# Kernel tuning notes

Measured on AMD Instinct MI355X. Metric: run time of the kernel, lower is better.

## Reference

```python
import jax, jax.numpy as jnp
import numpy as np


def _gcn_layer(x, W, b, src, dst, n_dst):
    """DGL GraphConv with norm='both': D_dst^{-1/2} A D_src^{-1/2} X W + b."""
    n_src = x.shape[0]
    ones = jnp.ones(src.shape[0], dtype=x.dtype)
    out_deg = jnp.clip(jax.ops.segment_sum(ones, src, num_segments=n_src), 1.0)
    in_deg = jnp.clip(jax.ops.segment_sum(ones, dst, num_segments=n_dst), 1.0)
    xn = x * (out_deg ** -0.5)[:, None]          # [n_src, F] source-side norm
    agg = jax.ops.segment_sum(xn[src], dst, num_segments=n_dst)  # sparse SpMM
    agg = agg * (in_deg ** -0.5)[:, None]        # dest-side norm
    return agg @ W + b


def setup_inputs() -> dict:
    key = jax.random.key(0)
    ks = jax.random.split(key, 9)
    N0, N1, N2 = 200000, 100000, 50000
    E1, E2 = 1600000, 800000
    F_in, F_hid, F_out = 128, 256, 128
    x = jax.random.normal(ks[0], (N0, F_in), dtype=jnp.float32)
    src1 = jax.random.randint(ks[1], (E1,), 0, N0, dtype=jnp.int32)
    dst1 = jax.random.randint(ks[2], (E1,), 0, N1, dtype=jnp.int32)
    src2 = jax.random.randint(ks[3], (E2,), 0, N1, dtype=jnp.int32)
    dst2 = jax.random.randint(ks[4], (E2,), 0, N2, dtype=jnp.int32)
    # Glorot-uniform weights like dgl GraphConv reset_parameters
    lim1 = (6.0 / (F_in + F_hid)) ** 0.5
    lim2 = (6.0 / (F_hid + F_out)) ** 0.5
    W1 = jax.random.uniform(ks[5], (F_in, F_hid), jnp.float32, -lim1, lim1)
    b1 = jnp.zeros((F_hid,), jnp.float32)
    W2 = jax.random.uniform(ks[6], (F_hid, F_out), jnp.float32, -lim2, lim2)
    b2 = jnp.zeros((F_out,), jnp.float32)
    return {"x": x, "W1": W1, "b1": b1, "W2": W2, "b2": b2,
            "src1": src1, "dst1": dst1, "src2": src2, "dst2": dst2,
            "n_dst1": N1, "n_dst2": N2}


def reference(x, W1, b1, W2, b2, src1, dst1, src2, dst2, n_dst1, n_dst2):
    h = jax.nn.relu(_gcn_layer(x, W1, b1, src1, dst1, n_dst1))
    out = jax.nn.relu(_gcn_layer(h, W2, b2, src2, dst2, n_dst2))
    return out
```

## Files before the change

kernel.cpp:

```cpp
#include <hip/hip_runtime.h>
#include <hip/hip_bf16.h>

#define F1 128
#define F2 256
#define F3 128
#define CAP 64

#define NB1D 391
#define NB2D 196
#define NB1S 782
#define NB2S 391
#define CAPD 4608
#define CAPS 2432
#define GD1 0
#define GD2 391
#define GS1 587
#define GS2 1369

typedef __attribute__((ext_vector_type(8))) short bf16x8;
typedef __attribute__((ext_vector_type(4))) float f32x4;
typedef __attribute__((ext_vector_type(4))) unsigned int u32x4;

__device__ inline float bf2f(unsigned short u) {
    return __uint_as_float(((unsigned int)u) << 16);
}
__device__ inline unsigned short f2bf(float f) {
    __hip_bfloat16 b = __float2bfloat16(f);
    return *reinterpret_cast<unsigned short*>(&b);
}
__device__ inline unsigned int pack2(float lo, float hi) {
    return ((unsigned int)f2bf(hi) << 16) | f2bf(lo);
}

#define ACC_ROW(u, c)                                   \
    acc[0] = fmaf(c, bf2f(u.x & 0xffff), acc[0]);       \
    acc[1] = fmaf(c, bf2f(u.x >> 16), acc[1]);          \
    acc[2] = fmaf(c, bf2f(u.y & 0xffff), acc[2]);       \
    acc[3] = fmaf(c, bf2f(u.y >> 16), acc[3]);          \
    acc[4] = fmaf(c, bf2f(u.z & 0xffff), acc[4]);       \
    acc[5] = fmaf(c, bf2f(u.z >> 16), acc[5]);          \
    acc[6] = fmaf(c, bf2f(u.w & 0xffff), acc[6]);       \
    acc[7] = fmaf(c, bf2f(u.w >> 16), acc[7]);

__global__ __launch_bounds__(1024) void scatter_build(
    const int* __restrict__ src1, const int* __restrict__ dst1,
    const int* __restrict__ src2, const int* __restrict__ dst2,
    const float* __restrict__ x, const float* __restrict__ W1,
    const float* __restrict__ W2, int* __restrict__ gcnt,
    unsigned int* __restrict__ bkt_d1, unsigned int* __restrict__ bkt_d2,
    unsigned char* __restrict__ bkt_s1, unsigned char* __restrict__ bkt_s2,
    unsigned int* __restrict__ xn, unsigned short* __restrict__ Bp1,
    unsigned short* __restrict__ Bp2, int E1, int E2, int A1, int A2, int B3) {
    __shared__ int hist[1184];
    int b = blockIdx.x, t = threadIdx.x;

    if (b < A1 + A2) {
        const int L1 = (b < A1);
        const int* __restrict__ src = L1 ? src1 : src2;
        const int* __restrict__ dst = L1 ? dst1 : dst2;
        const int E = L1 ? E1 : E2;
        const int NBd = L1 ? NB1D : NB2D;
        const int NBs = L1 ? NB1S : NB2S;
        int* gd = gcnt + (L1 ? GD1 : GD2);
        int* gs = gcnt + (L1 ? GS1 : GS2);
        unsigned int* bd = L1 ? bkt_d1 : bkt_d2;
        unsigned char* bs = L1 ? bkt_s1 : bkt_s2;
        int* hd = hist;
        int* hs = hist + NBd;
        for (int i = t; i < NBd + NBs; i += 1024) hist[i] = 0;
        __syncthreads();
        int e0 = (L1 ? b : b - A1) * 8192;
        int se[8], de[8];
#pragma unroll
        for (int i = 0; i < 8; ++i) {
            int e = e0 + i * 1024 + t;
            se[i] = -1;
            de[i] = -1;
            if (e < E) {
                int s = src[e], d = dst[e];
                se[i] = s;
                de[i] = d;
                atomicAdd(&hd[d >> 8], 1);
                atomicAdd(&hs[s >> 8], 1);
            }
        }
        __syncthreads();
        for (int i = t; i < NBd; i += 1024) {
            int c = hd[i];
            hd[i] = c ? atomicAdd(&gd[i], c) : 0;
        }
        for (int i = t; i < NBs; i += 1024) {
            int c = hs[i];
            hs[i] = c ? atomicAdd(&gs[i], c) : 0;
        }
        __syncthreads();
#pragma unroll
        for (int i = 0; i < 8; ++i) {
            if (de[i] >= 0) {
                int s = se[i], d = de[i];
                int pd = atomicAdd(&hd[d >> 8], 1);
                if (pd < CAPD)
                    bd[(size_t)(d >> 8) * CAPD + pd] = ((unsigned int)s << 8) | (d & 255);
                int ps = atomicAdd(&hs[s >> 8], 1);
                if (ps < CAPS)
                    bs[(size_t)(s >> 8) * CAPS + ps] = (unsigned char)(s & 255);
            }
        }
    } else if (b < A1 + A2 + B3) {
        size_t tid = (size_t)(b - A1 - A2) * 1024 + t;
        const f32x4* xp = (const f32x4*)x;
        f32x4 a = __builtin_nontemporal_load(xp + tid * 2);
        f32x4 c = __builtin_nontemporal_load(xp + tid * 2 + 1);
        u32x4 o;
        o.x = pack2(a.x, a.y);
        o.y = pack2(a.z, a.w);
        o.z = pack2(c.x, c.y);
        o.w = pack2(c.z, c.w);
        ((u32x4*)xn)[tid] = o;
    } else {
        int w = b - (A1 + A2 + B3);
        int which = w >> 5;
        const float* W = which ? W2 : W1;
        unsigned short* out = which ? Bp2 : Bp1;
        int N = which ? F3 : F2;
        int idx = (w & 31) * 1024 + t;
        int k = idx / N, n = idx % N;
        unsigned short v = f2bf(W[idx]);
        int kt = k >> 5, q = (k >> 3) & 3, j = k & 7;
        int nt = n >> 4, lane = q * 16 + (n & 15);
        int NT = N >> 4;
        out[(((kt * NT + nt) * 64 + lane) << 3) + j] = v;
    }
}

__global__ __launch_bounds__(256) void bucket_build(
    const int* __restrict__ gcnt,
    const unsigned int* __restrict__ bkt_d1, const unsigned int* __restrict__ bkt_d2,
    const unsigned char* __restrict__ bkt_s1, const unsigned char* __restrict__ bkt_s2,
    int* __restrict__ csr1, int* __restrict__ cnt_in1, float* __restrict__ rs_in1,
    int* __restrict__ csr2, int* __restrict__ cnt_in2, float* __restrict__ rs_in2,
    float* __restrict__ rs_out1, float* __restrict__ rs_out2) {
    __shared__ int hist[256];
    int b = blockIdx.x, t = threadIdx.x;
    hist[t] = 0;
    __syncthreads();

    if (b < NB1D + NB2D) {
        const int L1 = (b < NB1D);
        int bb = L1 ? b : b - NB1D;
        const unsigned int* bkt = L1 ? bkt_d1 : bkt_d2;
        int* csr = L1 ? csr1 : csr2;
        int* cnt_in = L1 ? cnt_in1 : cnt_in2;
        float* rs_in = L1 ? rs_in1 : rs_in2;
        int Nd = L1 ? 100000 : 50000;
        int n = gcnt[(L1 ? GD1 : GD2) + bb];
        if (n > CAPD) n = CAPD;
        size_t base = (size_t)bb * CAPD;
        for (int i = t; i < n; i += 256) {
            unsigned int v = bkt[base + i];
            int d = v & 255, s = (int)(v >> 8);
            int pos = atomicAdd(&hist[d], 1);
            if (pos < CAP) csr[((size_t)(bb * 256 + d)) * CAP + pos] = s;
        }
        __syncthreads();
        int node = bb * 256 + t;
        if (node < Nd) {
            int c = hist[t];
            cnt_in[node] = c < CAP ? c : CAP;
            rs_in[node] = rsqrtf((float)(c < 1 ? 1 : c));
        }
    } else {
        const int L1 = (b < NB1D + NB2D + NB1S);
        int bb = L1 ? b - (NB1D + NB2D) : b - (NB1D + NB2D + NB1S);
        const unsigned char* bkt = L1 ? bkt_s1 : bkt_s2;
        float* rs_out = L1 ? rs_out1 : rs_out2;
        int Ns = L1 ? 200000 : 100000;
        int n = gcnt[(L1 ? GS1 : GS2) + bb];
        if (n > CAPS) n = CAPS;
        size_t base = (size_t)bb * CAPS;
        for (int i = t; i < n; i += 256) atomicAdd(&hist[bkt[base + i]], 1);
        __syncthreads();
        int node = bb * 256 + t;
        if (node < Ns) rs_out[node] = rsqrtf((float)(hist[t] < 1 ? 1 : hist[t]));
    }
}

__global__ __launch_bounds__(256) void agg128_kernel(
    const unsigned int* __restrict__ X, const int* __restrict__ csr,
    const int* __restrict__ cnt, const float* __restrict__ rs_src,
    unsigned int* __restrict__ out, int ndst) {
    int wave = (int)((blockIdx.x * blockDim.x + threadIdx.x) >> 6);
    int lane = threadIdx.x & 63;
    if (wave >= ndst) return;
    size_t base = (size_t)wave * CAP;
    int len = cnt[wave];
    int sl = 0;
    float clv = 0.f;
    if (lane < len) {
        sl = csr[base + lane];
        clv = rs_src[sl];
    }
    int eg = lane >> 4, fs = lane & 15;
    float acc[8];
#pragma unroll
    for (int i = 0; i < 8; ++i) acc[i] = 0.f;
    for (int j = 0; j < len; j += 16) {
        int jA = j + eg, jB = j + 4 + eg, jC = j + 8 + eg, jD = j + 12 + eg;
        int sA = __shfl(sl, jA);
        int sB = __shfl(sl, jB);
        int sC = __shfl(sl, jC);
        int sD = __shfl(sl, jD);
        float cA = __shfl(clv, jA);
        float cB = __shfl(clv, jB);
        float cC = __shfl(clv, jC);
        float cD = __shfl(clv, jD);
        u32x4 uA = *(const u32x4*)(X + (size_t)sA * 64 + (fs << 2));
        u32x4 uB = *(const u32x4*)(X + (size_t)sB * 64 + (fs << 2));
        u32x4 uC = *(const u32x4*)(X + (size_t)sC * 64 + (fs << 2));
        u32x4 uD = *(const u32x4*)(X + (size_t)sD * 64 + (fs << 2));
        ACC_ROW(uA, cA)
        ACC_ROW(uB, cB)
        ACC_ROW(uC, cC)
        ACC_ROW(uD, cD)
    }
#pragma unroll
    for (int i = 0; i < 8; ++i) {
        acc[i] += __shfl_xor(acc[i], 16);
        acc[i] += __shfl_xor(acc[i], 32);
    }
    if (eg == 0) {
        u32x4 o;
        o.x = pack2(acc[0], acc[1]);
        o.y = pack2(acc[2], acc[3]);
        o.z = pack2(acc[4], acc[5]);
        o.w = pack2(acc[6], acc[7]);
        *((u32x4*)(out + (size_t)wave * 64) + fs) = o;
    }
}

__global__ __launch_bounds__(512) void gemm12(
    const unsigned short* __restrict__ A,
    const unsigned short* __restrict__ Bp1,
    const unsigned short* __restrict__ Bp2,
    const float* __restrict__ rs1, const float* __restrict__ rs2,
    const float* __restrict__ bias1,
    unsigned short* __restrict__ Y, int M) {
    __shared__ unsigned short Bs[32768];
    __shared__ unsigned short tmp[128][264];
    int lane = threadIdx.x & 63, wid = threadIdx.x >> 6;
    int t = threadIdx.x;
    int row0 = blockIdx.x * 128 + wid * 16;
    int q = lane >> 4, col = lane & 15;

#pragma unroll
    for (int i = 0; i < 8; ++i)
        ((u32x4*)Bs)[i * 512 + t] = ((const u32x4*)Bp1)[i * 512 + t];
    __syncthreads();

    int mload = row0 + col;
    if (mload > M - 1) mload = M - 1;
    const unsigned short* Arow = A + (size_t)mload * F1 + q * 8;
    f32x4 acc[16];
#pragma unroll
    for (int i = 0; i < 16; ++i) acc[i] = (f32x4){0.f, 0.f, 0.f, 0.f};
#pragma unroll
    for (int kt = 0; kt < 4; ++kt) {
        bf16x8 a = *(const bf16x8*)(Arow + kt * 32);
#pragma unroll
        for (int nt = 0; nt < 16; ++nt) {
            bf16x8 b = *(const bf16x8*)(Bs + (((kt * 16 + nt) * 64 + lane) << 3));
            acc[nt] = __builtin_amdgcn_mfma_f32_16x16x32_bf16(a, b, acc[nt], 0, 0, 0);
        }
    }
#pragma unroll
    for (int r = 0; r < 4; ++r) {
        int lrow = wid * 16 + q * 4 + r;
        int m = row0 + q * 4 + r;
        int mc = m < M ? m : M - 1;
        float s1 = rs1[mc], s2 = rs2[mc];
#pragma unroll
        for (int nt = 0; nt < 16; ++nt) {
            float v = fmaxf(fmaf(acc[nt][r], s1, bias1[nt * 16 + col]), 0.f) * s2;
            tmp[lrow][nt * 16 + col] = f2bf(v);
        }
    }
    __syncthreads();

#pragma unroll
    for (int i = 0; i < 8; ++i)
        ((u32x4*)Bs)[i * 512 + t] = ((const u32x4*)Bp2)[i * 512 + t];
    __syncthreads();

    f32x4 acc2[8];
#pragma unroll
    for (int i = 0; i < 8; ++i) acc2[i] = (f32x4){0.f, 0.f, 0.f, 0.f};
    const unsigned short* trow = &tmp[wid * 16 + col][q * 8];
#pragma unroll
    for (int kt = 0; kt < 8; ++kt) {
        bf16x8 a = *(const bf16x8*)(trow + kt * 32);
#pragma unroll
        for (int nt = 0; nt < 8; ++nt) {
            bf16x8 b = *(const bf16x8*)(Bs + (((kt * 8 + nt) * 64 + lane) << 3));
            acc2[nt] = __builtin_amdgcn_mfma_f32_16x16x32_bf16(a, b, acc2[nt], 0, 0, 0);
        }
    }
#pragma unroll
    for (int r = 0; r < 4; ++r) {
        int m = row0 + q * 4 + r;
        if (m >= M) continue;
#pragma unroll
        for (int nt = 0; nt < 8; ++nt)
            Y[(size_t)m * F3 + nt * 16 + col] = f2bf(acc2[nt][r]);
    }
}

__global__ __launch_bounds__(256) void agg_final(
    const unsigned int* __restrict__ Yv, const int* __restrict__ csr,
    const int* __restrict__ cnt, const float* __restrict__ rs_dst,
    const float* __restrict__ b2, float* __restrict__ out, int ndst) {
    int wave = (int)((blockIdx.x * blockDim.x + threadIdx.x) >> 6);
    int lane = threadIdx.x & 63;
    if (wave >= ndst) return;
    size_t base = (size_t)wave * CAP;
    int len = cnt[wave];
    int sl = 0;
    float clv = 0.f;
    if (lane < len) {
        sl = csr[base + lane];
        clv = 1.f;
    }
    int eg = lane >> 4, fs = lane & 15;
    float acc[8];
#pragma unroll
    for (int i = 0; i < 8; ++i) acc[i] = 0.f;
    for (int j = 0; j < len; j += 16) {
        int jA = j + eg, jB = j + 4 + eg, jC = j + 8 + eg, jD = j + 12 + eg;
        int sA = __shfl(sl, jA);
        int sB = __shfl(sl, jB);
        int sC = __shfl(sl, jC);
        int sD = __shfl(sl, jD);
        float cA = __shfl(clv, jA);
        float cB = __shfl(clv, jB);
        float cC = __shfl(clv, jC);
        float cD = __shfl(clv, jD);
        u32x4 uA = *(const u32x4*)(Yv + (size_t)sA * 64 + (fs << 2));
        u32x4 uB = *(const u32x4*)(Yv + (size_t)sB * 64 + (fs << 2));
        u32x4 uC = *(const u32x4*)(Yv + (size_t)sC * 64 + (fs << 2));
        u32x4 uD = *(const u32x4*)(Yv + (size_t)sD * 64 + (fs << 2));
        ACC_ROW(uA, cA)
        ACC_ROW(uB, cB)
        ACC_ROW(uC, cC)
        ACC_ROW(uD, cD)
    }
#pragma unroll
    for (int i = 0; i < 8; ++i) {
        acc[i] += __shfl_xor(acc[i], 16);
        acc[i] += __shfl_xor(acc[i], 32);
    }
    if (eg < 2) {
        float sc = rs_dst[wave];
        f32x4 bias = ((const f32x4*)b2)[(fs << 1) | eg];
        float v0 = eg ? acc[4] : acc[0];
        float v1 = eg ? acc[5] : acc[1];
        float v2 = eg ? acc[6] : acc[2];
        float v3 = eg ? acc[7] : acc[3];
        f32x4 o;
        o.x = fmaxf(fmaf(v0, sc, bias.x), 0.f);
        o.y = fmaxf(fmaf(v1, sc, bias.y), 0.f);
        o.z = fmaxf(fmaf(v2, sc, bias.z), 0.f);
        o.w = fmaxf(fmaf(v3, sc, bias.w), 0.f);
        __builtin_nontemporal_store(o, (f32x4*)out + (size_t)wave * 32 + (fs << 1) + eg);
    }
}

extern "C" void kernel_launch(void* const* d_in, const int* in_sizes, int n_in,
                              void* d_out, int out_size, void* d_ws, size_t ws_size,
                              hipStream_t stream) {
    const float* x  = (const float*)d_in[0];
    const float* W1 = (const float*)d_in[1];
    const float* b1 = (const float*)d_in[2];
    const float* W2 = (const float*)d_in[3];
    const float* b2 = (const float*)d_in[4];
    const int* src1 = (const int*)d_in[5];
    const int* dst1 = (const int*)d_in[6];
    const int* src2 = (const int*)d_in[7];
    const int* dst2 = (const int*)d_in[8];
    const int E1 = in_sizes[5], E2 = in_sizes[7];
    const int N0 = in_sizes[0] / F1;
    const int N1 = 100000, N2 = 50000;

    char* p = (char*)d_ws;
    int* gcnt = (int*)p; p += 2048 * 4;
    float* rs_out1 = (float*)p; p += (size_t)N0 * 4;
    float* rs_in1  = (float*)p; p += (size_t)N1 * 4;
    float* rs_out2 = (float*)p; p += (size_t)N1 * 4;
    float* rs_in2  = (float*)p; p += (size_t)N2 * 4;
    int* cnt_in1 = (int*)p; p += (size_t)N1 * 4;
    int* cnt_in2 = (int*)p; p += (size_t)N2 * 4;
    unsigned int* bkt_d1 = (unsigned int*)p; p += (size_t)NB1D * CAPD * 4;
    unsigned int* bkt_d2 = (unsigned int*)p; p += (size_t)NB2D * CAPD * 4;
    unsigned char* bkt_s1 = (unsigned char*)p; p += (size_t)NB1S * CAPS;
    unsigned char* bkt_s2 = (unsigned char*)p; p += (size_t)NB2S * CAPS;
    int* csr1 = (int*)p; p += (size_t)N1 * CAP * 4;
    int* csr2 = (int*)p; p += (size_t)N2 * CAP * 4;
    unsigned short* Bp1 = (unsigned short*)p; p += (size_t)F1 * F2 * 2;
    unsigned short* Bp2 = (unsigned short*)p; p += (size_t)F2 * F3 * 2;
    unsigned short* xn  = (unsigned short*)p; p += (size_t)N0 * F1 * 2;
    unsigned short* agg = (unsigned short*)p; p += (size_t)N1 * F1 * 2;
    unsigned short* y = xn;

    (void)hipMemsetAsync(gcnt, 0, 2048 * 4, stream);

    int A1 = (E1 + 8191) / 8192;
    int A2 = (E2 + 8191) / 8192;
    int B3 = N0 * F1 / 8 / 1024;
    scatter_build<<<A1 + A2 + B3 + 64, 1024, 0, stream>>>(
        src1, dst1, src2, dst2, x, W1, W2, gcnt,
        bkt_d1, bkt_d2, bkt_s1, bkt_s2,
        (unsigned int*)xn, Bp1, Bp2, E1, E2, A1, A2, B3);

    bucket_build<<<NB1D + NB2D + NB1S + NB2S, 256, 0, stream>>>(
        gcnt, bkt_d1, bkt_d2, bkt_s1, bkt_s2,
        csr1, cnt_in1, rs_in1, csr2, cnt_in2, rs_in2, rs_out1, rs_out2);

    agg128_kernel<<<(N1 + 3) / 4, 256, 0, stream>>>((const unsigned int*)xn, csr1,
                                                    cnt_in1, rs_out1,
                                                    (unsigned int*)agg, N1);

    gemm12<<<(N1 + 127) / 128, 512, 0, stream>>>(agg, Bp1, Bp2, rs_in1, rs_out2, b1, y, N1);

    agg_final<<<(N2 + 3) / 4, 256, 0, stream>>>((const unsigned int*)y, csr2, cnt_in2,
                                                rs_in2, b2, (float*)d_out, N2);
}
```

Measured before the change: 363.0 us.

## Build CSR directly with global atomics, drop bucket pass and precomputed norms

Replaces the two-pass bucketed graph build (shared-memory histograms, global bucket buffers, then a second bucket_build kernel) with a single pass that does per-node global atomicAdd for in-count, out-degree, and the CSR slot. Degree normalisation factors are now computed on the fly with rsqrtf from the raw integer counts inside the aggregation and GEMM kernels, so no rs_* arrays are written. agg_final points padded lanes at a zero row (row N1 of y, which gemm12 now zero-fills) instead of using a zero coefficient. This removes one kernel launch and the bucket round trip, but relies on heavily contended, scattered global atomics and random 4-byte CSR writes.

```diff
diff --git a/kernel.cpp b/kernel.cpp
--- a/kernel.cpp
+++ b/kernel.cpp
@@ -6,16 +6,7 @@
 #define F3 128
 #define CAP 64
 
-#define NB1D 391
-#define NB2D 196
-#define NB1S 782
-#define NB2S 391
-#define CAPD 4608
-#define CAPS 2432
-#define GD1 0
-#define GD2 391
-#define GS1 587
-#define GS2 1369
+#define YPAD 100096
 
 typedef __attribute__((ext_vector_type(8))) short bf16x8;
 typedef __attribute__((ext_vector_type(4))) float f32x4;
@@ -30,6 +21,9 @@
 }
 __device__ inline unsigned int pack2(float lo, float hi) {
     return ((unsigned int)f2bf(hi) << 16) | f2bf(lo);
+}
+__device__ inline float rsdeg(int c) {
+    return rsqrtf((float)(c < 1 ? 1 : c));
 }
 
 #define ACC_ROW(u, c)                                   \
@@ -42,16 +36,26 @@
     acc[6] = fmaf(c, bf2f(u.w & 0xffff), acc[6]);       \
     acc[7] = fmaf(c, bf2f(u.w >> 16), acc[7]);
 
+#define ACC_ROW_ADD(u)                          \
+    acc[0] += bf2f(u.x & 0xffff);               \
+    acc[1] += bf2f(u.x >> 16);                  \
+    acc[2] += bf2f(u.y & 0xffff);               \
+    acc[3] += bf2f(u.y >> 16);                  \
+    acc[4] += bf2f(u.z & 0xffff);               \
+    acc[5] += bf2f(u.z >> 16);                  \
+    acc[6] += bf2f(u.w & 0xffff);               \
+    acc[7] += bf2f(u.w >> 16);
+
 __global__ __launch_bounds__(1024) void scatter_build(
     const int* __restrict__ src1, const int* __restrict__ dst1,
     const int* __restrict__ src2, const int* __restrict__ dst2,
     const float* __restrict__ x, const float* __restrict__ W1,
-    const float* __restrict__ W2, int* __restrict__ gcnt,
-    unsigned int* __restrict__ bkt_d1, unsigned int* __restrict__ bkt_d2,
-    unsigned char* __restrict__ bkt_s1, unsigned char* __restrict__ bkt_s2,
+    const float* __restrict__ W2,
+    int* __restrict__ cnt1, int* __restrict__ outdeg1,
+    int* __restrict__ cnt2, int* __restrict__ outdeg2,
+    int* __restrict__ csr1, int* __restrict__ csr2,
     unsigned int* __restrict__ xn, unsigned short* __restrict__ Bp1,
     unsigned short* __restrict__ Bp2, int E1, int E2, int A1, int A2, int B3) {
-    __shared__ int hist[1184];
     int b = blockIdx.x, t = threadIdx.x;
 
     if (b < A1 + A2) {
@@ -59,51 +63,18 @@
         const int* __restrict__ src = L1 ? src1 : src2;
         const int* __restrict__ dst = L1 ? dst1 : dst2;
         const int E = L1 ? E1 : E2;
-        const int NBd = L1 ? NB1D : NB2D;
-        const int NBs = L1 ? NB1S : NB2S;
-        int* gd = gcnt + (L1 ? GD1 : GD2);
-        int* gs = gcnt + (L1 ? GS1 : GS2);
-        unsigned int* bd = L1 ? bkt_d1 : bkt_d2;
-        unsigned char* bs = L1 ? bkt_s1 : bkt_s2;
-        int* hd = hist;
-        int* hs = hist + NBd;
-        for (int i = t; i < NBd + NBs; i += 1024) hist[i] = 0;
-        __syncthreads();
+        int* cnt = L1 ? cnt1 : cnt2;
+        int* od  = L1 ? outdeg1 : outdeg2;
+        int* csr = L1 ? csr1 : csr2;
         int e0 = (L1 ? b : b - A1) * 8192;
-        int se[8], de[8];
-#pragma unroll
-        for (int i = 0; i < 8; ++i) {
-            int e = e0 + i * 1024 + t;
-            se[i] = -1;
-            de[i] = -1;
+#pragma unroll
+        for (int k = 0; k < 8; ++k) {
+            int e = e0 + k * 1024 + t;
             if (e < E) {
                 int s = src[e], d = dst[e];
-                se[i] = s;
-                de[i] = d;
-                atomicAdd(&hd[d >> 8], 1);
-                atomicAdd(&hs[s >> 8], 1);
-            }
-        }
-        __syncthreads();
-        for (int i = t; i < NBd; i += 1024) {
-            int c = hd[i];
-            hd[i] = c ? atomicAdd(&gd[i], c) : 0;
-        }
-        for (int i = t; i < NBs; i += 1024) {
-            int c = hs[i];
-            hs[i] = c ? atomicAdd(&gs[i], c) : 0;
-        }
-        __syncthreads();
-#pragma unroll
-        for (int i = 0; i < 8; ++i) {
-            if (de[i] >= 0) {
-                int s = se[i], d = de[i];
-                int pd = atomicAdd(&hd[d >> 8], 1);
-                if (pd < CAPD)
-                    bd[(size_t)(d >> 8) * CAPD + pd] = ((unsigned int)s << 8) | (d & 255);
-                int ps = atomicAdd(&hs[s >> 8], 1);
-                if (ps < CAPS)
-                    bs[(size_t)(s >> 8) * CAPS + ps] = (unsigned char)(s & 255);
+                atomicAdd(&od[s], 1);
+                int pos = atomicAdd(&cnt[d], 1);
+                if (pos < CAP) csr[(size_t)d * CAP + pos] = s;
             }
         }
     } else if (b < A1 + A2 + B3) {
@@ -133,72 +104,21 @@
     }
 }
 
-__global__ __launch_bounds__(256) void bucket_build(
-    const int* __restrict__ gcnt,
-    const unsigned int* __restrict__ bkt_d1, const unsigned int* __restrict__ bkt_d2,
-    const unsigned char* __restrict__ bkt_s1, const unsigned char* __restrict__ bkt_s2,
-    int* __restrict__ csr1, int* __restrict__ cnt_in1, float* __restrict__ rs_in1,
-    int* __restrict__ csr2, int* __restrict__ cnt_in2, float* __restrict__ rs_in2,
-    float* __restrict__ rs_out1, float* __restrict__ rs_out2) {
-    __shared__ int hist[256];
-    int b = blockIdx.x, t = threadIdx.x;
-    hist[t] = 0;
-    __syncthreads();
-
-    if (b < NB1D + NB2D) {
-        const int L1 = (b < NB1D);
-        int bb = L1 ? b : b - NB1D;
-        const unsigned int* bkt = L1 ? bkt_d1 : bkt_d2;
-        int* csr = L1 ? csr1 : csr2;
-        int* cnt_in = L1 ? cnt_in1 : cnt_in2;
-        float* rs_in = L1 ? rs_in1 : rs_in2;
-        int Nd = L1 ? 100000 : 50000;
-        int n = gcnt[(L1 ? GD1 : GD2) + bb];
-        if (n > CAPD) n = CAPD;
-        size_t base = (size_t)bb * CAPD;
-        for (int i = t; i < n; i += 256) {
-            unsigned int v = bkt[base + i];
-            int d = v & 255, s = (int)(v >> 8);
-            int pos = atomicAdd(&hist[d], 1);
-            if (pos < CAP) csr[((size_t)(bb * 256 + d)) * CAP + pos] = s;
-        }
-        __syncthreads();
-        int node = bb * 256 + t;
-        if (node < Nd) {
-            int c = hist[t];
-            cnt_in[node] = c < CAP ? c : CAP;
-            rs_in[node] = rsqrtf((float)(c < 1 ? 1 : c));
-        }
-    } else {
-        const int L1 = (b < NB1D + NB2D + NB1S);
-        int bb = L1 ? b - (NB1D + NB2D) : b - (NB1D + NB2D + NB1S);
-        const unsigned char* bkt = L1 ? bkt_s1 : bkt_s2;
-        float* rs_out = L1 ? rs_out1 : rs_out2;
-        int Ns = L1 ? 200000 : 100000;
-        int n = gcnt[(L1 ? GS1 : GS2) + bb];
-        if (n > CAPS) n = CAPS;
-        size_t base = (size_t)bb * CAPS;
-        for (int i = t; i < n; i += 256) atomicAdd(&hist[bkt[base + i]], 1);
-        __syncthreads();
-        int node = bb * 256 + t;
-        if (node < Ns) rs_out[node] = rsqrtf((float)(hist[t] < 1 ? 1 : hist[t]));
-    }
-}
-
 __global__ __launch_bounds__(256) void agg128_kernel(
     const unsigned int* __restrict__ X, const int* __restrict__ csr,
-    const int* __restrict__ cnt, const float* __restrict__ rs_src,
+    const int* __restrict__ cnt, const int* __restrict__ od_src,
     unsigned int* __restrict__ out, int ndst) {
     int wave = (int)((blockIdx.x * blockDim.x + threadIdx.x) >> 6);
     int lane = threadIdx.x & 63;
     if (wave >= ndst) return;
     size_t base = (size_t)wave * CAP;
     int len = cnt[wave];
+    if (len > CAP) len = CAP;
     int sl = 0;
     float clv = 0.f;
     if (lane < len) {
         sl = csr[base + lane];
-        clv = rs_src[sl];
+        clv = rsdeg(od_src[sl]);
     }
     int eg = lane >> 4, fs = lane & 15;
     float acc[8];
@@ -242,7 +162,7 @@
     const unsigned short* __restrict__ A,
     const unsigned short* __restrict__ Bp1,
     const unsigned short* __restrict__ Bp2,
-    const float* __restrict__ rs1, const float* __restrict__ rs2,
+    const int* __restrict__ cnt_in, const int* __restrict__ od2,
     const float* __restrict__ bias1,
     unsigned short* __restrict__ Y, int M) {
     __shared__ unsigned short Bs[32768];
@@ -268,8 +188,8 @@
         bf16x8 a = *(const bf16x8*)(Arow + kt * 32);
 #pragma unroll
         for (int nt = 0; nt < 16; ++nt) {
-            bf16x8 b = *(const bf16x8*)(Bs + (((kt * 16 + nt) * 64 + lane) << 3));
-            acc[nt] = __builtin_amdgcn_mfma_f32_16x16x32_bf16(a, b, acc[nt], 0, 0, 0);
+            bf16x8 bfr = *(const bf16x8*)(Bs + (((kt * 16 + nt) * 64 + lane) << 3));
+            acc[nt] = __builtin_amdgcn_mfma_f32_16x16x32_bf16(a, bfr, acc[nt], 0, 0, 0);
         }
     }
 #pragma unroll
@@ -277,7 +197,7 @@
         int lrow = wid * 16 + q * 4 + r;
         int m = row0 + q * 4 + r;
         int mc = m < M ? m : M - 1;
-        float s1 = rs1[mc], s2 = rs2[mc];
+        float s1 = rsdeg(cnt_in[mc]), s2 = rsdeg(od2[mc]);
 #pragma unroll
         for (int nt = 0; nt < 16; ++nt) {
             float v = fmaxf(fmaf(acc[nt][r], s1, bias1[nt * 16 + col]), 0.f) * s2;
@@ -300,35 +220,32 @@
         bf16x8 a = *(const bf16x8*)(trow + kt * 32);
 #pragma unroll
         for (int nt = 0; nt < 8; ++nt) {
-            bf16x8 b = *(const bf16x8*)(Bs + (((kt * 8 + nt) * 64 + lane) << 3));
-            acc2[nt] = __builtin_amdgcn_mfma_f32_16x16x32_bf16(a, b, acc2[nt], 0, 0, 0);
+            bf16x8 bfr = *(const bf16x8*)(Bs + (((kt * 8 + nt) * 64 + lane) << 3));
+            acc2[nt] = __builtin_amdgcn_mfma_f32_16x16x32_bf16(a, bfr, acc2[nt], 0, 0, 0);
         }
     }
 #pragma unroll
     for (int r = 0; r < 4; ++r) {
         int m = row0 + q * 4 + r;
-        if (m >= M) continue;
+        int live = m < M;
 #pragma unroll
         for (int nt = 0; nt < 8; ++nt)
-            Y[(size_t)m * F3 + nt * 16 + col] = f2bf(acc2[nt][r]);
+            Y[(size_t)m * F3 + nt * 16 + col] = live ? f2bf(acc2[nt][r]) : (unsigned short)0;
     }
 }
 
 __global__ __launch_bounds__(256) void agg_final(
     const unsigned int* __restrict__ Yv, const int* __restrict__ csr,
-    const int* __restrict__ cnt, const float* __restrict__ rs_dst,
-    const float* __restrict__ b2, float* __restrict__ out, int ndst) {
+    const int* __restrict__ cnt, const float* __restrict__ b2,
+    float* __restrict__ out, int ndst, int zrow) {
     int wave = (int)((blockIdx.x * blockDim.x + threadIdx.x) >> 6);
     int lane = threadIdx.x & 63;
     if (wave >= ndst) return;
     size_t base = (size_t)wave * CAP;
-    int len = cnt[wave];
-    int sl = 0;
-    float clv = 0.f;
-    if (lane < len) {
-        sl = csr[base + lane];
-        clv = 1.f;
-    }
+    int craw = cnt[wave];
+    int len = craw < CAP ? craw : CAP;
+    int sl = zrow;
+    if (lane < len) sl = csr[base + lane];
     int eg = lane >> 4, fs = lane & 15;
     float acc[8];
 #pragma unroll
@@ -339,18 +256,14 @@
         int sB = __shfl(sl, jB);
         int sC = __shfl(sl, jC);
         int sD = __shfl(sl, jD);
-        float cA = __shfl(clv, jA);
-        float cB = __shfl(clv, jB);
-        float cC = __shfl(clv, jC);
-        float cD = __shfl(clv, jD);
         u32x4 uA = *(const u32x4*)(Yv + (size_t)sA * 64 + (fs << 2));
         u32x4 uB = *(const u32x4*)(Yv + (size_t)sB * 64 + (fs << 2));
         u32x4 uC = *(const u32x4*)(Yv + (size_t)sC * 64 + (fs << 2));
         u32x4 uD = *(const u32x4*)(Yv + (size_t)sD * 64 + (fs << 2));
-        ACC_ROW(uA, cA)
-        ACC_ROW(uB, cB)
-        ACC_ROW(uC, cC)
-        ACC_ROW(uD, cD)
+        ACC_ROW_ADD(uA)
+        ACC_ROW_ADD(uB)
+        ACC_ROW_ADD(uC)
+        ACC_ROW_ADD(uD)
     }
 #pragma unroll
     for (int i = 0; i < 8; ++i) {
@@ -358,7 +271,7 @@
         acc[i] += __shfl_xor(acc[i], 32);
     }
     if (eg < 2) {
-        float sc = rs_dst[wave];
+        float sc = rsdeg(craw);
         f32x4 bias = ((const f32x4*)b2)[(fs << 1) | eg];
         float v0 = eg ? acc[4] : acc[0];
         float v1 = eg ? acc[5] : acc[1];
@@ -390,17 +303,11 @@
     const int N1 = 100000, N2 = 50000;
 
     char* p = (char*)d_ws;
-    int* gcnt = (int*)p; p += 2048 * 4;
-    float* rs_out1 = (float*)p; p += (size_t)N0 * 4;
-    float* rs_in1  = (float*)p; p += (size_t)N1 * 4;
-    float* rs_out2 = (float*)p; p += (size_t)N1 * 4;
-    float* rs_in2  = (float*)p; p += (size_t)N2 * 4;
-    int* cnt_in1 = (int*)p; p += (size_t)N1 * 4;
-    int* cnt_in2 = (int*)p; p += (size_t)N2 * 4;
-    unsigned int* bkt_d1 = (unsigned int*)p; p += (size_t)NB1D * CAPD * 4;
-    unsigned int* bkt_d2 = (unsigned int*)p; p += (size_t)NB2D * CAPD * 4;
-    unsigned char* bkt_s1 = (unsigned char*)p; p += (size_t)NB1S * CAPS;
-    unsigned char* bkt_s2 = (unsigned char*)p; p += (size_t)NB2S * CAPS;
+    int* cnt1    = (int*)p; p += (size_t)N1 * 4;
+    int* outdeg1 = (int*)p; p += (size_t)N0 * 4;
+    int* cnt2    = (int*)p; p += (size_t)N2 * 4;
+    int* outdeg2 = (int*)p; p += (size_t)N1 * 4;
+    size_t cnt_bytes = ((size_t)N1 + N0 + N2 + N1) * 4;
     int* csr1 = (int*)p; p += (size_t)N1 * CAP * 4;
     int* csr2 = (int*)p; p += (size_t)N2 * CAP * 4;
     unsigned short* Bp1 = (unsigned short*)p; p += (size_t)F1 * F2 * 2;
@@ -409,26 +316,22 @@
     unsigned short* agg = (unsigned short*)p; p += (size_t)N1 * F1 * 2;
     unsigned short* y = xn;
 
-    (void)hipMemsetAsync(gcnt, 0, 2048 * 4, stream);
+    (void)hipMemsetAsync(cnt1, 0, cnt_bytes, stream);
 
     int A1 = (E1 + 8191) / 8192;
     int A2 = (E2 + 8191) / 8192;
     int B3 = N0 * F1 / 8 / 1024;
     scatter_build<<<A1 + A2 + B3 + 64, 1024, 0, stream>>>(
-        src1, dst1, src2, dst2, x, W1, W2, gcnt,
-        bkt_d1, bkt_d2, bkt_s1, bkt_s2,
+        src1, dst1, src2, dst2, x, W1, W2,
+        cnt1, outdeg1, cnt2, outdeg2, csr1, csr2,
         (unsigned int*)xn, Bp1, Bp2, E1, E2, A1, A2, B3);
 
-    bucket_build<<<NB1D + NB2D + NB1S + NB2S, 256, 0, stream>>>(
-        gcnt, bkt_d1, bkt_d2, bkt_s1, bkt_s2,
-        csr1, cnt_in1, rs_in1, csr2, cnt_in2, rs_in2, rs_out1, rs_out2);
-
     agg128_kernel<<<(N1 + 3) / 4, 256, 0, stream>>>((const unsigned int*)xn, csr1,
-                                                    cnt_in1, rs_out1,
+                                                    cnt1, outdeg1,
                                                     (unsigned int*)agg, N1);
 
-    gemm12<<<(N1 + 127) / 128, 512, 0, stream>>>(agg, Bp1, Bp2, rs_in1, rs_out2, b1, y, N1);
-
-    agg_final<<<(N2 + 3) / 4, 256, 0, stream>>>((const unsigned int*)y, csr2, cnt_in2,
-                                                rs_in2, b2, (float*)d_out, N2);
-}
+    gemm12<<<(N1 + 127) / 128, 512, 0, stream>>>(agg, Bp1, Bp2, cnt1, outdeg2, b1, y, N1);
+
+    agg_final<<<(N2 + 3) / 4, 256, 0, stream>>>((const unsigned int*)y, csr2, cnt2,
+                                                b2, (float*)d_out, N2, N1);
+}
```

Result: slower. 557.9 us (+53.7%).
